# Kernel tuning notes

Hardware: AMD Instinct MI355X
Metric: run time of the kernel (lower is better)

Reference implementation:

```python
import jax, jax.numpy as jnp
import numpy as np

K = 32
EPS = 1e-5  # BatchNorm eps; eval mode with running_mean=0, running_var=1


def knn_idx(x):
    # x: [B, C, N] -> idx of K nearest neighbors [B, N, K]
    inner = -2.0 * jnp.einsum('bcn,bcm->bnm', x, x)
    xx = jnp.sum(x * x, axis=1)  # [B, N]
    pd = -xx[:, :, None] - inner - xx[:, None, :]  # negative squared dist
    return jax.lax.top_k(pd, K)[1]


def get_neighbors(x):
    # x: [B, C, N] -> edge features [B, N, K, 2C] (nbr - ctr, ctr)
    idx = knn_idx(x)
    xt = jnp.transpose(x, (0, 2, 1))  # [B, N, C]
    nbrs = jax.vmap(lambda p, i: p[i])(xt, idx)  # [B, N, K, C]
    ctr = jnp.broadcast_to(xt[:, :, None, :], nbrs.shape)
    return jnp.concatenate([nbrs - ctr, ctr], axis=-1)


def bn_eval(h, g, b, nd):
    # inference-mode BN, running_mean=0, running_var=1
    shape = [1, -1] + [1] * (nd - 2)
    return h * (g / jnp.sqrt(1.0 + EPS)).reshape(shape) + b.reshape(shape)


def edge_conv(x, W, g, b):
    # x: [B, C, N] -> [B, O, N]; 1x1 conv over edge feats + BN + LeakyReLU + max over K
    feat = get_neighbors(x)  # [B, N, K, 2C]
    h = jnp.einsum('bnkc,oc->bonk', feat, W)
    h = jax.nn.leaky_relu(bn_eval(h, g, b, 4), 0.2)
    return jnp.max(h, axis=-1)


def setup_inputs():
    key = jax.random.key(0)
    ks = jax.random.split(key, 40)
    B, N = 4, 2048

    def rn(i, shape, s=0.1):
        return jax.random.normal(ks[i], shape, jnp.float32) * s

    def gm(i, c):
        return 1.0 + rn(i, (c,))

    inp = {
        'x': jax.random.normal(ks[0], (B, 3, N), jnp.float32),
        'l': jax.random.normal(ks[1], (B, 5), jnp.float32),
        'n': jax.random.normal(ks[2], (B, 7), jnp.float32),
        'W1': rn(3, (64, 6)), 'g1': gm(4, 64), 'b1': rn(5, (64,)),
        'W2': rn(6, (64, 128)), 'g2': gm(7, 64), 'b2': rn(8, (64,)),
        'W3': rn(9, (128, 128)), 'g3': gm(10, 128), 'b3': rn(11, (128,)),
        'W4': rn(12, (256, 256)), 'g4': gm(13, 256), 'b4': rn(14, (256,)),
        'W5': rn(15, (1024, 512)), 'g5': gm(16, 1024), 'b5': rn(17, (1024,)),
        'W6': rn(18, (64, 5)), 'g6': gm(19, 64), 'b6': rn(20, (64,)),
        'W7': rn(21, (64, 7)), 'g7': gm(22, 64), 'b7': rn(23, (64,)),
        'L1': rn(24, (512, 1152)), 'g8': gm(25, 512), 'b8': rn(26, (512,)),
        'L2': rn(27, (256, 512)), 'L2b': rn(28, (256,)), 'g9': gm(29, 256), 'b9': rn(30, (256,)),
        'L3': rn(31, (28, 256)), 'L3b': rn(32, (28,)),
    }
    return inp


def reference(x, l, n, W1, g1, b1, W2, g2, b2, W3, g3, b3, W4, g4, b4,
              W5, g5, b5, W6, g6, b6, W7, g7, b7,
              L1, g8, b8, L2, L2b, g9, b9, L3, L3b):
    x1 = edge_conv(x, W1, g1, b1)    # [B, 64, N]
    x2 = edge_conv(x1, W2, g2, b2)   # [B, 64, N]
    x3 = edge_conv(x2, W3, g3, b3)   # [B, 128, N]
    x4 = edge_conv(x3, W4, g4, b4)   # [B, 256, N]
    cat = jnp.concatenate([x1, x2, x3, x4], axis=1)  # [B, 512, N]
    h = jnp.einsum('bcn,oc->bon', cat, W5)
    h = jax.nn.leaky_relu(bn_eval(h, g5, b5, 3), 0.2)
    h = jnp.max(h, axis=-1)  # global max pool -> [B, 1024]
    lf = jax.nn.leaky_relu(bn_eval(jnp.einsum('bc,oc->bo', l, W6), g6, b6, 2), 0.2)
    nf = jax.nn.leaky_relu(bn_eval(jnp.einsum('bc,oc->bo', n, W7), g7, b7, 2), 0.2)
    v = jnp.concatenate([h, lf, nf], axis=-1)  # [B, 1152]
    v = jax.nn.relu(bn_eval(v @ L1.T, g8, b8, 2))  # dropout = identity (eval)
    v = jax.nn.relu(bn_eval(v @ L2.T + L2b, g9, b9, 2))
    return v @ L3.T + L3b  # [B, 28]
```

## Files before the change

kernel.cpp:

```cpp
#include <hip/hip_runtime.h>
#include <hip/hip_bf16.h>

#define NPTS 2048
#define NB 4
#define KNN 32
#define NIN 33

static __device__ __forceinline__ float b2f(__hip_bfloat16 v) { return __bfloat162float(v); }
#define ISQ 0.99999499996875f

typedef __attribute__((ext_vector_type(8))) short short8v;
typedef __attribute__((ext_vector_type(4))) float f32x4;

static __device__ __forceinline__ unsigned ordkey(float f) {
  unsigned u = __float_as_uint(f);
  return u ^ (unsigned)(((int)u >> 31) | 0x80000000);
}

static __device__ __forceinline__ void loadv(const float* p, float (&d)[1]) { d[0] = *p; }
static __device__ __forceinline__ void loadv(const float* p, float (&d)[2]) {
  float2 v = *(const float2*)p; d[0] = v.x; d[1] = v.y;
}
static __device__ __forceinline__ void loadv(const float* p, float (&d)[4]) {
  float4 v = *(const float4*)p; d[0] = v.x; d[1] = v.y; d[2] = v.z; d[3] = v.w;
}

static __device__ __forceinline__ float wave_red_sum(float s) {
#pragma unroll
  for (int off = 32; off > 0; off >>= 1) s += __shfl_xor(s, off);
  return s;
}

__global__ __launch_bounds__(64) void detect_kernel(const unsigned short* __restrict__ x,
                                                    int* __restrict__ flag) {
  int cnt = 0;
  for (int i = threadIdx.x; i < 512; i += 64) {
    unsigned e = (x[i] >> 7) & 0xFFu;
    if (e >= 0xC6u) cnt++;
  }
#pragma unroll
  for (int off = 32; off > 0; off >>= 1) cnt += __shfl_down(cnt, off);
  if (threadIdx.x == 0) flag[0] = (cnt == 0) ? 1 : 0;
}

struct CvtArgs {
  const void* src[NIN];
  int off[NIN + 1];
};

__global__ __launch_bounds__(256) void cvt_all_kernel(CvtArgs a, float* __restrict__ out,
                                                      int total, int nb1,
                                                      __hip_bfloat16* __restrict__ w5bf,
                                                      const int* __restrict__ flag) {
  if ((int)blockIdx.x < nb1) {
    int t = blockIdx.x * 256 + threadIdx.x;
    if (t >= total) return;
    int s = 0;
    while (t >= a.off[s + 1]) s++;
    int j = t - a.off[s];
    float v;
    if (flag[0]) v = b2f(((const __hip_bfloat16*)a.src[s])[j]);
    else         v = ((const float*)a.src[s])[j];
    out[t] = v;
  } else {
    int t = (blockIdx.x - nb1) * 256 + threadIdx.x;
    if (flag[0]) w5bf[t] = ((const __hip_bfloat16*)a.src[15])[t];
    else         w5bf[t] = __float2bfloat16(((const float*)a.src[15])[t]);
  }
}

template <int C>
__global__ __launch_bounds__(256) void xx_kernel(const float* __restrict__ x, long bstride,
                                                 float* __restrict__ xx) {
  int t = blockIdx.x * 256 + threadIdx.x;
  int b = t / NPTS, m = t % NPTS;
  const float* xb = x + (long)b * bstride + m;
  float s = 0.f;
#pragma unroll
  for (int c = 0; c < C; ++c) { float v = xb[(long)c * NPTS]; s = fmaf(v, v, s); }
  xx[t] = s;
}

template <int C>
__global__ __launch_bounds__(256) void pdgemmsym_kernel(const float* __restrict__ x, long bstride,
                                                        const float* __restrict__ xx,
                                                        unsigned* __restrict__ keys) {
  constexpr int KT = (C < 16) ? C : 16;
  __shared__ __align__(16) float At[KT][64];
  __shared__ __align__(16) float Bt[KT][64];
  __shared__ __align__(16) unsigned Ts[64][68];
  int t = blockIdx.x;
  int tj = (int)((sqrtf(8.f * (float)t + 1.f) - 1.f) * 0.5f);
  while ((tj + 1) * (tj + 2) / 2 <= t) tj++;
  while (tj * (tj + 1) / 2 > t) tj--;
  int ti = t - tj * (tj + 1) / 2;
  int n0 = ti * 64, m0 = tj * 64;
  int tid = threadIdx.x, tx = tid & 15, ty = tid >> 4;
  const float* xb = x + (long)blockIdx.y * bstride;
  float acc[4][4] = {};
  for (int k0 = 0; k0 < C; k0 += KT) {
    for (int lin = tid; lin < KT * 64; lin += 256) {
      int r = lin >> 6, col = lin & 63;
      At[r][col] = xb[(long)(k0 + r) * NPTS + n0 + col];
      Bt[r][col] = xb[(long)(k0 + r) * NPTS + m0 + col];
    }
    __syncthreads();
#pragma unroll
    for (int kc = 0; kc < KT; ++kc) {
      float4 av = *(const float4*)&At[kc][ty * 4];
      float4 bv = *(const float4*)&Bt[kc][tx * 4];
      acc[0][0] = fmaf(av.x, bv.x, acc[0][0]); acc[0][1] = fmaf(av.x, bv.y, acc[0][1]);
      acc[0][2] = fmaf(av.x, bv.z, acc[0][2]); acc[0][3] = fmaf(av.x, bv.w, acc[0][3]);
      acc[1][0] = fmaf(av.y, bv.x, acc[1][0]); acc[1][1] = fmaf(av.y, bv.y, acc[1][1]);
      acc[1][2] = fmaf(av.y, bv.z, acc[1][2]); acc[1][3] = fmaf(av.y, bv.w, acc[1][3]);
      acc[2][0] = fmaf(av.z, bv.x, acc[2][0]); acc[2][1] = fmaf(av.z, bv.y, acc[2][1]);
      acc[2][2] = fmaf(av.z, bv.z, acc[2][2]); acc[2][3] = fmaf(av.z, bv.w, acc[2][3]);
      acc[3][0] = fmaf(av.w, bv.x, acc[3][0]); acc[3][1] = fmaf(av.w, bv.y, acc[3][1]);
      acc[3][2] = fmaf(av.w, bv.z, acc[3][2]); acc[3][3] = fmaf(av.w, bv.w, acc[3][3]);
    }
    __syncthreads();
  }
  const float* xxq = xx + (long)blockIdx.y * NPTS;
  float4 xxm = *(const float4*)&xxq[m0 + tx * 4];
  unsigned* kb = keys + ((long)blockIdx.y << 22);
  unsigned ok[4][4];
#pragma unroll
  for (int i = 0; i < 4; ++i) {
    float xxn = xxq[n0 + ty * 4 + i];
    ok[i][0] = ordkey((-xxn - (-2.f * acc[i][0])) - xxm.x);
    ok[i][1] = ordkey((-xxn - (-2.f * acc[i][1])) - xxm.y);
    ok[i][2] = ordkey((-xxn - (-2.f * acc[i][2])) - xxm.z);
    ok[i][3] = ordkey((-xxn - (-2.f * acc[i][3])) - xxm.w);
    uint4 o = make_uint4(ok[i][0], ok[i][1], ok[i][2], ok[i][3]);
    *(uint4*)&kb[(long)(n0 + ty * 4 + i) * NPTS + m0 + tx * 4] = o;
  }
  if (ti != tj) {
#pragma unroll
    for (int i = 0; i < 4; ++i)
#pragma unroll
      for (int j = 0; j < 4; ++j) Ts[tx * 4 + j][ty * 4 + i] = ok[i][j];
    __syncthreads();
#pragma unroll
    for (int i = 0; i < 4; ++i)
      *(uint4*)&kb[(long)(m0 + ty * 4 + i) * NPTS + n0 + tx * 4] =
          *(const uint4*)&Ts[ty * 4 + i][tx * 4];
  }
}

__global__ __launch_bounds__(256) void select_kernel(const unsigned* __restrict__ keys,
                                                     int* __restrict__ idxout) {
  int wave = threadIdx.x >> 6, lane = threadIdx.x & 63;
  int q = blockIdx.x * 4 + wave;
  int bloc = q >> 11, n = q & 2047;
  const uint4* rp = (const uint4*)(keys + ((long)((bloc << 11) | n) << 11));
  unsigned K[32];
#pragma unroll
  for (int t = 0; t < 8; ++t) {
    uint4 kk = rp[t * 64 + lane];
    K[4 * t + 0] = kk.x; K[4 * t + 1] = kk.y; K[4 * t + 2] = kk.z; K[4 * t + 3] = kk.w;
  }
  unsigned orv = K[0], andv = K[0];
#pragma unroll
  for (int s = 1; s < 32; ++s) { orv |= K[s]; andv &= K[s]; }
#pragma unroll
  for (int xm = 32; xm >= 1; xm >>= 1) {
    orv  |= __shfl_xor(orv, xm);
    andv &= __shfl_xor(andv, xm);
  }
  unsigned V = orv ^ andv;
  unsigned P = 0;
  int need = KNN;
  for (int b = 31; b >= 0; --b) {
    unsigned bit = 1u << b;
    if (!(V & bit)) { P |= (andv & bit); continue; }
    unsigned hm = 0xFFFFFFFFu << b;
    unsigned Pb = P | bit;
    int c = 0;
#pragma unroll
    for (int s = 0; s < 32; ++s) c += ((K[s] & hm) == Pb) ? 1 : 0;
#pragma unroll
    for (int xm = 32; xm >= 1; xm >>= 1) c += __shfl_xor(c, xm);
    if (c >= need) P = Pb;
    else need -= c;
  }
  int* orow = idxout + ((bloc << 11) | n) * KNN;
  int base = 0;
  unsigned eqmask = 0;
#pragma unroll
  for (int s = 0; s < 32; ++s) {
    bool take = K[s] > P;
    unsigned long long bal = __ballot(take);
    if (take) {
      int pos = base + (int)__popcll(bal & ((1ull << lane) - 1ull));
      orow[pos] = ((s >> 2) << 8) + lane * 4 + (s & 3);
    }
    base += (int)__popcll(bal);
    if (K[s] == P) eqmask |= (1u << s);
  }
  int rem = KNN - base;
  for (int it = 0; it < rem; ++it) {
    unsigned mym = 0xFFFFFFFFu;
    if (eqmask) {
      int s = __ffs(eqmask) - 1;
      mym = (unsigned)(((s >> 2) << 8) + lane * 4 + (s & 3));
    }
    unsigned wm = mym;
#pragma unroll
    for (int xm = 32; xm >= 1; xm >>= 1) {
      unsigned o = __shfl_xor(wm, xm);
      wm = o < wm ? o : wm;
    }
    if (mym == wm) {
      orow[base + it] = (int)wm;
      eqmask &= eqmask - 1;
    }
  }
}

template <int C>
__global__ __launch_bounds__(256) void yzt_kernel(const float* __restrict__ x, long bstride,
                                                  const float* __restrict__ W, int O,
                                                  float* __restrict__ yt, float* __restrict__ zt) {
  constexpr int KT = (C < 16) ? C : 16;
  __shared__ __align__(16) float Xs[KT][64];
  __shared__ __align__(16) float Wy[KT][64];
  __shared__ __align__(16) float Wp[KT][64];
  int b = blockIdx.z, m0 = blockIdx.y * 64, o0 = blockIdx.x * 64;
  int tid = threadIdx.x, tx = tid & 15, ty = tid >> 4;
  const float* xb = x + (long)b * bstride;
  const int twoC = 2 * C;
  float accy[4][4] = {}, accp[4][4] = {};
  for (int k0 = 0; k0 < C; k0 += KT) {
    for (int lin = tid; lin < KT * 64; lin += 256) {
      int r = lin >> 6, col = lin & 63;
      Xs[r][col] = xb[(long)(k0 + r) * NPTS + m0 + col];
      float wy = W[(o0 + col) * twoC + k0 + r];
      Wy[r][col] = wy;
      Wp[r][col] = W[(o0 + col) * twoC + C + k0 + r] - wy;
    }
    __syncthreads();
#pragma unroll
    for (int kc = 0; kc < KT; ++kc) {
      float4 wv = *(const float4*)&Wy[kc][tx * 4];
      float4 pv = *(const float4*)&Wp[kc][tx * 4];
      float xm[4];
      xm[0] = Xs[kc][ty * 4 + 0]; xm[1] = Xs[kc][ty * 4 + 1];
      xm[2] = Xs[kc][ty * 4 + 2]; xm[3] = Xs[kc][ty * 4 + 3];
#pragma unroll
      for (int i = 0; i < 4; ++i) {
        accy[i][0] = fmaf(xm[i], wv.x, accy[i][0]);
        accy[i][1] = fmaf(xm[i], wv.y, accy[i][1]);
        accy[i][2] = fmaf(xm[i], wv.z, accy[i][2]);
        accy[i][3] = fmaf(xm[i], wv.w, accy[i][3]);
        accp[i][0] = fmaf(xm[i], pv.x, accp[i][0]);
        accp[i][1] = fmaf(xm[i], pv.y, accp[i][1]);
        accp[i][2] = fmaf(xm[i], pv.z, accp[i][2]);
        accp[i][3] = fmaf(xm[i], pv.w, accp[i][3]);
      }
    }
    __syncthreads();
  }
#pragma unroll
  for (int i = 0; i < 4; ++i) {
    long base = ((long)b * NPTS + m0 + ty * 4 + i) * O + o0 + tx * 4;
    *(float4*)&yt[base] = make_float4(accy[i][0], accy[i][1], accy[i][2], accy[i][3]);
    *(float4*)&zt[base] = make_float4(accp[i][0], accp[i][1], accp[i][2], accp[i][3]);
  }
}

template <int RO>
__global__ __launch_bounds__(256) void gmaxt_kernel(const float* __restrict__ yt,
                                                    const float* __restrict__ zt,
                                                    const int* __restrict__ idx,
                                                    const float* __restrict__ g,
                                                    const float* __restrict__ bb,
                                                    float* __restrict__ out, long obstride,
                                                    float* __restrict__ xxout,
                                                    __hip_bfloat16* __restrict__ catbf, int loff) {
  constexpr int O = RO * 64;
  int wave = threadIdx.x >> 6, lane = threadIdx.x & 63;
  int n = blockIdx.x * 4 + wave, b = blockIdx.y;
  int jreg = idx[((b << 11) + n) * KNN + (lane & 31)];
  int obase = lane * RO;
  float gs[RO], bs[RO], zr[RO], acc[RO];
  loadv(zt + ((long)(b << 11) + n) * O + obase, zr);
#pragma unroll
  for (int r = 0; r < RO; ++r) {
    gs[r] = g[obase + r] * ISQ;
    bs[r] = bb[obase + r];
    acc[r] = -INFINITY;
  }
  const float* yb = yt + ((long)(b << 11)) * O + obase;
#pragma unroll
  for (int k = 0; k < KNN; ++k) {
    int j = __shfl(jreg, k);
    float yv[RO];
    loadv(yb + (long)j * O, yv);
#pragma unroll
    for (int r = 0; r < RO; ++r) {
      float v = fmaf(gs[r], yv[r] + zr[r], bs[r]);
      v = v >= 0.f ? v : 0.2f * v;
      acc[r] = fmaxf(acc[r], v);
    }
  }
  float* op = out + (long)b * obstride + (long)obase * NPTS + n;
#pragma unroll
  for (int r = 0; r < RO; ++r) op[(long)r * NPTS] = acc[r];
  __hip_bfloat16* cb = catbf + ((long)(b << 11) + n) * 512 + loff + obase;
#pragma unroll
  for (int r = 0; r < RO; ++r) cb[r] = __float2bfloat16(acc[r]);
  if (xxout) {
    float ss = 0.f;
#pragma unroll
    for (int r = 0; r < RO; ++r) ss = fmaf(acc[r], acc[r], ss);
    ss = wave_red_sum(ss);
    if (lane == 0) xxout[(b << 11) + n] = ss;
  }
}

__global__ __launch_bounds__(256) void gemm5m_kernel(const __hip_bfloat16* __restrict__ catbf,
                                                     const __hip_bfloat16* __restrict__ w5bf,
                                                     const float* __restrict__ g5,
                                                     const float* __restrict__ b5,
                                                     float* __restrict__ pmax) {
  int b = blockIdx.z, po0 = blockIdx.y * 128, n0 = blockIdx.x * 64;
  int wave = threadIdx.x >> 6, lane = threadIdx.x & 63;
  int quad = lane >> 4, l15 = lane & 15;
  const short* wp0 = (const short*)w5bf + (long)(po0 + wave * 32 + l15) * 512 + quad * 8;
  const short* wp1 = wp0 + 16 * 512;
  const short* cp = (const short*)catbf + ((long)(b << 11) + n0 + l15) * 512 + quad * 8;
  f32x4 acc[2][4] = {};
  short8v ca0 = *(const short8v*)wp0;
  short8v ca1 = *(const short8v*)wp1;
  short8v cb[4];
#pragma unroll
  for (int nt = 0; nt < 4; ++nt) cb[nt] = *(const short8v*)(cp + nt * 16 * 512);
  for (int k0 = 0; k0 < 512; k0 += 32) {
    int kn = (k0 + 32 < 512) ? k0 + 32 : 0;
    short8v na0 = *(const short8v*)(wp0 + kn);
    short8v na1 = *(const short8v*)(wp1 + kn);
    short8v nb[4];
#pragma unroll
    for (int nt = 0; nt < 4; ++nt) nb[nt] = *(const short8v*)(cp + nt * 16 * 512 + kn);
#pragma unroll
    for (int nt = 0; nt < 4; ++nt) {
      acc[0][nt] = __builtin_amdgcn_mfma_f32_16x16x32_bf16(ca0, cb[nt], acc[0][nt], 0, 0, 0);
      acc[1][nt] = __builtin_amdgcn_mfma_f32_16x16x32_bf16(ca1, cb[nt], acc[1][nt], 0, 0, 0);
    }
    ca0 = na0; ca1 = na1;
#pragma unroll
    for (int nt = 0; nt < 4; ++nt) cb[nt] = nb[nt];
  }
#pragma unroll
  for (int i = 0; i < 2; ++i) {
#pragma unroll
    for (int r = 0; r < 4; ++r) {
      int po = po0 + wave * 32 + i * 16 + quad * 4 + r;
      float sc = g5[po] * ISQ;
      float bi = b5[po];
      float mx = -INFINITY;
#pragma unroll
      for (int nt = 0; nt < 4; ++nt) {
        float v = fmaf(sc, acc[i][nt][r], bi);
        v = v >= 0.f ? v : 0.2f * v;
        mx = fmaxf(mx, v);
      }
#pragma unroll
      for (int xm = 1; xm < 16; xm <<= 1) mx = fmaxf(mx, __shfl_xor(mx, xm));
      if (l15 == 0) pmax[(long)(b * 1024 + po) * 32 + blockIdx.x] = mx;
    }
  }
}

__global__ __launch_bounds__(256) void redlfnf_kernel(const float* __restrict__ pmax,
                                                      const float* __restrict__ l,
                                                      const float* __restrict__ nn,
                                                      const float* __restrict__ W6,
                                                      const float* __restrict__ g6,
                                                      const float* __restrict__ b6,
                                                      const float* __restrict__ W7,
                                                      const float* __restrict__ g7,
                                                      const float* __restrict__ b7,
                                                      float* __restrict__ v) {
  if (blockIdx.x < 16) {
    int t = blockIdx.x * 256 + threadIdx.x;
    float mx = -INFINITY;
#pragma unroll
    for (int j = 0; j < 32; ++j) mx = fmaxf(mx, pmax[(long)t * 32 + j]);
    int b = t >> 10, po = t & 1023;
    v[b * 1152 + po] = mx;
  } else {
    int idx = (blockIdx.x - 16) * 256 + threadIdx.x;
    int b = idx >> 7, t = idx & 127;
    if (t < 64) {
      float s = 0.f;
#pragma unroll
      for (int c = 0; c < 5; ++c) s = fmaf(W6[t * 5 + c], l[b * 5 + c], s);
      float val = fmaf(g6[t] * ISQ, s, b6[t]);
      v[b * 1152 + 1024 + t] = val >= 0.f ? val : 0.2f * val;
    } else {
      int o = t - 64;
      float s = 0.f;
#pragma unroll
      for (int c = 0; c < 7; ++c) s = fmaf(W7[o * 7 + c], nn[b * 7 + c], s);
      float val = fmaf(g7[o] * ISQ, s, b7[o]);
      v[b * 1152 + 1088 + o] = val >= 0.f ? val : 0.2f * val;
    }
  }
}

__global__ __launch_bounds__(256) void head1_kernel(const float* __restrict__ v,
                                                    const float* __restrict__ L1,
                                                    const float* __restrict__ g8,
                                                    const float* __restrict__ b8,
                                                    float* __restrict__ v1) {
  int wave = threadIdx.x >> 6, lane = threadIdx.x & 63;
  int t = blockIdx.x * 4 + wave;
  int b = t >> 9, o = t & 511;
  const float* vb = v + b * 1152;
  const float* wr = L1 + (long)o * 1152;
  float s = 0.f;
#pragma unroll
  for (int c = lane; c < 1152; c += 64) s = fmaf(wr[c], vb[c], s);
  s = wave_red_sum(s);
  if (lane == 0) {
    float val = fmaf(g8[o] * ISQ, s, b8[o]);
    v1[t] = fmaxf(val, 0.f);
  }
}

__global__ __launch_bounds__(256) void head2_kernel(const float* __restrict__ v1,
                                                    const float* __restrict__ L2,
                                                    const float* __restrict__ L2b,
                                                    const float* __restrict__ g9,
                                                    const float* __restrict__ b9,
                                                    float* __restrict__ v2) {
  int wave = threadIdx.x >> 6, lane = threadIdx.x & 63;
  int t = blockIdx.x * 4 + wave;
  int b = t >> 8, o = t & 255;
  const float* vb = v1 + b * 512;
  const float* wr = L2 + (long)o * 512;
  float s = 0.f;
#pragma unroll
  for (int c = lane; c < 512; c += 64) s = fmaf(wr[c], vb[c], s);
  s = wave_red_sum(s);
  if (lane == 0) {
    float sv = s + L2b[o];
    float val = fmaf(g9[o] * ISQ, sv, b9[o]);
    v2[t] = fmaxf(val, 0.f);
  }
}

__global__ __launch_bounds__(256) void head3_kernel(const float* __restrict__ v2,
                                                    const float* __restrict__ L3,
                                                    const float* __restrict__ L3b,
                                                    void* __restrict__ out,
                                                    const int* __restrict__ flag) {
  int wave = threadIdx.x >> 6, lane = threadIdx.x & 63;
  int t = blockIdx.x * 4 + wave;
  if (t >= 112) return;
  int b = t / 28, o = t % 28;
  const float* vb = v2 + b * 256;
  const float* wr = L3 + o * 256;
  float s = 0.f;
#pragma unroll
  for (int c = lane; c < 256; c += 64) s = fmaf(wr[c], vb[c], s);
  s = wave_red_sum(s);
  if (lane == 0) {
    float sv = s + L3b[o];
    if (flag[0]) ((__hip_bfloat16*)out)[t] = __float2bfloat16(sv);
    else         ((float*)out)[t] = sv;
  }
}

extern "C" void kernel_launch(void* const* d_in, const int* in_sizes, int n_in,
                              void* d_out, int out_size, void* d_ws, size_t ws_size,
                              hipStream_t stream) {
  CvtArgs ca;
  int off[NIN + 1];
  off[0] = 0;
  for (int i = 0; i < NIN; ++i) {
    ca.src[i] = d_in[i];
    off[i + 1] = off[i] + in_sizes[i];
    ca.off[i] = off[i];
  }
  ca.off[NIN] = off[NIN];
  const int total = off[NIN];

  int* flag = (int*)d_ws;
  float* fin = (float*)((char*)d_ws + 64);
  const float* xf  = fin + off[0];
  const float* lf  = fin + off[1];
  const float* nf  = fin + off[2];
  const float* W1f = fin + off[3];  const float* g1f = fin + off[4];  const float* b1f = fin + off[5];
  const float* W2f = fin + off[6];  const float* g2f = fin + off[7];  const float* b2f_ = fin + off[8];
  const float* W3f = fin + off[9];  const float* g3f = fin + off[10]; const float* b3f = fin + off[11];
  const float* W4f = fin + off[12]; const float* g4f = fin + off[13]; const float* b4f = fin + off[14];
  const float* g5f = fin + off[16]; const float* b5f = fin + off[17];
  const float* W6f = fin + off[18]; const float* g6f = fin + off[19]; const float* b6f = fin + off[20];
  const float* W7f = fin + off[21]; const float* g7f = fin + off[22]; const float* b7f = fin + off[23];
  const float* L1f = fin + off[24]; const float* g8f = fin + off[25]; const float* b8f = fin + off[26];
  const float* L2f = fin + off[27]; const float* L2bf = fin + off[28];
  const float* g9f = fin + off[29]; const float* b9f = fin + off[30];
  const float* L3f = fin + off[31]; const float* L3bf = fin + off[32];

  float* p = fin + ((total + 15) & ~15);
  float* cat  = p;
  float* yb   = cat + 4 * 512 * NPTS;
  float* zb   = yb + 4 * 256 * NPTS;
  float* xxb  = zb + 4 * 256 * NPTS;
  int*   idxb = (int*)(xxb + 4 * NPTS);
  float* pmax = (float*)(idxb + 4 * NPTS * KNN);
  float* vb   = pmax + 4 * 1024 * 32;
  float* v1b  = vb + 4 * 1152;
  float* v2b  = v1b + 4 * 512;
  __hip_bfloat16* w5bf  = (__hip_bfloat16*)(v2b + 4 * 256);
  __hip_bfloat16* catbf = w5bf + 1024 * 512;
  unsigned* keys_tail = (unsigned*)(catbf + (size_t)4 * NPTS * 512);

  size_t need_full = (size_t)((char*)(keys_tail + (size_t)NB * NPTS * NPTS) - (char*)d_ws);
  int bpass = (ws_size >= need_full) ? NB : 1;
  unsigned* keys = (bpass == NB) ? keys_tail : (unsigned*)yb;

  const long bst1 = 3L * NPTS;
  const long bstc = 512L * NPTS;
  const int NTRI = 32 * 33 / 2;
  const int nb1 = (total + 255) / 256;

  detect_kernel<<<1, 64, 0, stream>>>((const unsigned short*)d_in[0], flag);
  cvt_all_kernel<<<nb1 + 2048, 256, 0, stream>>>(ca, fin, total, nb1, w5bf, flag);

  xx_kernel<3><<<32, 256, 0, stream>>>(xf, bst1, xxb);
  for (int b0 = 0; b0 < NB; b0 += bpass) {
    pdgemmsym_kernel<3><<<dim3(NTRI, bpass), 256, 0, stream>>>(xf + b0 * bst1, bst1, xxb + b0 * NPTS, keys);
    select_kernel<<<512 * bpass, 256, 0, stream>>>(keys, idxb + (long)b0 * NPTS * KNN);
  }
  yzt_kernel<3><<<dim3(1, 32, NB), 256, 0, stream>>>(xf, bst1, W1f, 64, yb, zb);
  gmaxt_kernel<1><<<dim3(512, NB), 256, 0, stream>>>(yb, zb, idxb, g1f, b1f, cat, bstc, xxb, catbf, 0);

  for (int b0 = 0; b0 < NB; b0 += bpass) {
    pdgemmsym_kernel<64><<<dim3(NTRI, bpass), 256, 0, stream>>>(cat + b0 * bstc, bstc, xxb + b0 * NPTS, keys);
    select_kernel<<<512 * bpass, 256, 0, stream>>>(keys, idxb + (long)b0 * NPTS * KNN);
  }
  yzt_kernel<64><<<dim3(1, 32, NB), 256, 0, stream>>>(cat, bstc, W2f, 64, yb, zb);
  gmaxt_kernel<1><<<dim3(512, NB), 256, 0, stream>>>(yb, zb, idxb, g2f, b2f_, cat + 64L * NPTS, bstc, xxb, catbf, 64);

  for (int b0 = 0; b0 < NB; b0 += bpass) {
    pdgemmsym_kernel<64><<<dim3(NTRI, bpass), 256, 0, stream>>>(cat + 64L * NPTS + b0 * bstc, bstc, xxb + b0 * NPTS, keys);
    select_kernel<<<512 * bpass, 256, 0, stream>>>(keys, idxb + (long)b0 * NPTS * KNN);
  }
  yzt_kernel<64><<<dim3(2, 32, NB), 256, 0, stream>>>(cat + 64L * NPTS, bstc, W3f, 128, yb, zb);
  gmaxt_kernel<2><<<dim3(512, NB), 256, 0, stream>>>(yb, zb, idxb, g3f, b3f, cat + 128L * NPTS, bstc, xxb, catbf, 128);

  for (int b0 = 0; b0 < NB; b0 += bpass) {
    pdgemmsym_kernel<128><<<dim3(NTRI, bpass), 256, 0, stream>>>(cat + 128L * NPTS + b0 * bstc, bstc, xxb + b0 * NPTS, keys);
    select_kernel<<<512 * bpass, 256, 0, stream>>>(keys, idxb + (long)b0 * NPTS * KNN);
  }
  yzt_kernel<128><<<dim3(4, 32, NB), 256, 0, stream>>>(cat + 128L * NPTS, bstc, W4f, 256, yb, zb);
  gmaxt_kernel<4><<<dim3(512, NB), 256, 0, stream>>>(yb, zb, idxb, g4f, b4f, cat + 256L * NPTS, bstc, (float*)nullptr, catbf, 256);

  gemm5m_kernel<<<dim3(32, 8, NB), 256, 0, stream>>>(catbf, w5bf, g5f, b5f, pmax);
  redlfnf_kernel<<<18, 256, 0, stream>>>(pmax, lf, nf, W6f, g6f, b6f, W7f, g7f, b7f, vb);

  head1_kernel<<<512, 256, 0, stream>>>(vb, L1f, g8f, b8f, v1b);
  head2_kernel<<<256, 256, 0, stream>>>(v1b, L2f, L2bf, g9f, b9f, v2b);
  head3_kernel<<<28, 256, 0, stream>>>(v2b, L3f, L3bf, d_out, flag);
}
```

Before: 628.4 us.

## Run top-k radix select on per-lane top-4 candidates with exact fallback

The select kernel now keeps each lane's four largest keys and runs the bitwise radix search for the 32nd-largest threshold over only those 256 candidates, counting with ballots instead of 32-element loops plus shuffle reductions. The result is then checked by counting keys above the threshold across all 32 per-lane keys. If the candidate set was insufficient, it falls back to the full radix search. This is meant to cut the per-bit counting cost in the common case, at the price of an extra verification pass and occasional full recomputation.

```diff
diff --git a/kernel.cpp b/kernel.cpp
--- a/kernel.cpp
+++ b/kernel.cpp
@@ -159,29 +159,67 @@
     uint4 kk = rp[t * 64 + lane];
     K[4 * t + 0] = kk.x; K[4 * t + 1] = kk.y; K[4 * t + 2] = kk.z; K[4 * t + 3] = kk.w;
   }
-  unsigned orv = K[0], andv = K[0];
-#pragma unroll
-  for (int s = 1; s < 32; ++s) { orv |= K[s]; andv &= K[s]; }
+  unsigned t0 = 0, t1 = 0, t2 = 0, t3 = 0;
+#pragma unroll
+  for (int s = 0; s < 32; ++s) {
+    unsigned k = K[s];
+    if (k > t3) {
+      if (k > t1) {
+        if (k > t0) { t3 = t2; t2 = t1; t1 = t0; t0 = k; }
+        else        { t3 = t2; t2 = t1; t1 = k; }
+      } else {
+        if (k > t2) { t3 = t2; t2 = k; }
+        else        { t3 = k; }
+      }
+    }
+  }
+  unsigned orv = t0 | t1 | t2 | t3, andv = t0 & t1 & t2 & t3;
 #pragma unroll
   for (int xm = 32; xm >= 1; xm >>= 1) {
     orv  |= __shfl_xor(orv, xm);
     andv &= __shfl_xor(andv, xm);
   }
   unsigned V = orv ^ andv;
-  unsigned P = 0;
+  unsigned P = andv & ~V;
   int need = KNN;
   for (int b = 31; b >= 0; --b) {
     unsigned bit = 1u << b;
-    if (!(V & bit)) { P |= (andv & bit); continue; }
+    if (!(V & bit)) continue;
     unsigned hm = 0xFFFFFFFFu << b;
-    unsigned Pb = P | bit;
-    int c = 0;
-#pragma unroll
-    for (int s = 0; s < 32; ++s) c += ((K[s] & hm) == Pb) ? 1 : 0;
-#pragma unroll
-    for (int xm = 32; xm >= 1; xm >>= 1) c += __shfl_xor(c, xm);
-    if (c >= need) P = Pb;
+    unsigned Pb = (P & hm) | bit;
+    int c = (int)__popcll(__ballot((t0 & hm) == Pb)) +
+            (int)__popcll(__ballot((t1 & hm) == Pb)) +
+            (int)__popcll(__ballot((t2 & hm) == Pb)) +
+            (int)__popcll(__ballot((t3 & hm) == Pb));
+    if (c >= need) P |= bit;
     else need -= c;
+  }
+  int cg = 0;
+#pragma unroll
+  for (int s = 0; s < 32; ++s) cg += (int)__popcll(__ballot(K[s] > P));
+  if (cg > KNN - 1) {
+    unsigned orf = K[0], anf = K[0];
+#pragma unroll
+    for (int s = 1; s < 32; ++s) { orf |= K[s]; anf &= K[s]; }
+#pragma unroll
+    for (int xm = 32; xm >= 1; xm >>= 1) {
+      orf |= __shfl_xor(orf, xm);
+      anf &= __shfl_xor(anf, xm);
+    }
+    unsigned Vf = orf ^ anf;
+    P = anf & ~Vf;
+    need = KNN;
+    for (int b = 31; b >= 0; --b) {
+      unsigned bit = 1u << b;
+      if (!(Vf & bit)) continue;
+      unsigned hm = 0xFFFFFFFFu << b;
+      unsigned Pb = (P & hm) | bit;
+      int c = 0;
+#pragma unroll
+      for (int s = 0; s < 32; ++s) c += (int)__popcll(__ballot((K[s] & hm) == Pb));
+      if (c >= need) P |= bit;
+      else need -= c;
+    }
   }
   int* orow = idxout + ((bloc << 11) | n) * KNN;
   int base = 0;
```

Measured after the change: 559.2 us. -11.0%, faster.
